# Kernel optimization log

Measured on AMD Instinct MI355X. Metric: run time of the kernel, lower is better.

Reference implementation:

```python
import jax, jax.numpy as jnp
import numpy as np

N_NODES = 100000
N_EDGES = 1000000
NHID = 128
N_CLASSES = 5000


def setup_inputs() -> dict:
    key = jax.random.key(0)
    ks = jax.random.split(key, 8)
    feature = jax.random.normal(ks[0], (N_NODES, NHID), dtype=jnp.float32)
    # Linear weights stored as [in, out] so forward is x @ W + b
    W1 = jax.random.normal(ks[1], (2 * NHID, NHID), dtype=jnp.float32) * (1.0 / np.sqrt(2 * NHID))
    b1 = jnp.zeros((NHID,), dtype=jnp.float32)
    alpha = jnp.full((NHID,), 0.25, dtype=jnp.float32)  # PReLU per-channel init
    W2 = jax.random.normal(ks[2], (NHID, 2), dtype=jnp.float32) * (1.0 / np.sqrt(NHID))
    b2 = jnp.zeros((2,), dtype=jnp.float32)
    row = jax.random.randint(ks[3], (N_EDGES,), 0, N_NODES, dtype=jnp.int64)
    col = jax.random.randint(ks[4], (N_EDGES,), 0, N_NODES, dtype=jnp.int64)
    label = jax.random.randint(ks[5], (N_NODES,), 0, N_CLASSES, dtype=jnp.int64)
    return {"feature": feature, "W1": W1, "b1": b1, "alpha": alpha,
            "W2": W2, "b2": b2, "row": row, "col": col, "label": label}


def reference(feature, W1, b1, alpha, W2, b2, row, col, label):
    # per-edge label: 1 if endpoints share a cluster label
    y = (label[row] == label[col]).astype(jnp.int32)  # [E]
    # edge gather + concat: [E, 2*nhid]
    x = jnp.concatenate([feature[row], feature[col]], axis=1)
    h = x @ W1 + b1                                   # [E, nhid]
    h = jnp.where(h >= 0, h, alpha * h)               # PReLU, per-channel alpha
    logits = h @ W2 + b2                              # [E, 2]
    logp = jax.nn.log_softmax(logits, axis=-1)
    # mean cross-entropy over edges
    loss = -jnp.mean(jnp.take_along_axis(logp, y[:, None], axis=1))
    return loss
```

## Files before the change

kernel.cpp:

```cpp
#include <hip/hip_runtime.h>
#include <hip/hip_bf16.h>

typedef __bf16 bf16_t;
typedef bf16_t bf16x8 __attribute__((ext_vector_type(8)));
typedef float floatx4 __attribute__((ext_vector_type(4)));
typedef float floatx2 __attribute__((ext_vector_type(2)));

#define N_NODES 100000
#define N_EDGES 1000000

#define NBK 98
#define NBP 104
#define NSEG 23
#define SEGCAP 512
#define BCAP (NSEG * SEGCAP)
#define SPCAP 32768
#define SCAT_BLKS 326
#define SCAT_WIN 3072

#define OFF_AUX   12800000
#define OFF_WT    14400000
#define OFF_WABS  14465536
#define OFF_W1G   14466048
#define OFF_CONST 14466560
#define OFF_RS    14466624ULL
#define OFF_SPILL 24264256ULL
#define OFF_CNT   24526400ULL
#define WS_NEED   24533120ULL
#define CNT_INTS  (NBP * 16 + 16)


__global__ __launch_bounds__(256) void k_prep(const float* __restrict__ W1,
                                              const float* __restrict__ b1,
                                              const float* __restrict__ alpha,
                                              const float* __restrict__ W2,
                                              const float* __restrict__ b2,
                                              bf16_t* __restrict__ WT,
                                              float* __restrict__ wabsp,
                                              float* __restrict__ w1g,
                                              float* __restrict__ constg,
                                              float* __restrict__ out,
                                              int* __restrict__ cnt,
                                              int zero_cnt) {
    const int t = threadIdx.x;
    if (blockIdx.x < 128) {
        int i = blockIdx.x * 256 + t;
        int n = i >> 7, k = i & 127;
        float v = (n < 128) ? W1[k * 128 + n] : W1[(k + 128) * 128 + (n - 128)];
        WT[i] = (bf16_t)v;
        return;
    }
    if (zero_cnt) {
        for (int i = t; i < CNT_INTS; i += 256) cnt[i] = 0;
    }
    __shared__ float w1L[128];
    if (t < 128) {
        float wd = W2[2 * t + 1] - W2[2 * t];
        float al = alpha[t];
        float w1v = wd * (1.f + al) * 0.5f;
        w1L[t] = w1v;
        w1g[t] = w1v;
        int col = (t & 64) + (t & 3) * 16 + ((t >> 2) & 15);
        float wdc = W2[2 * col + 1] - W2[2 * col];
        wabsp[t] = wdc * (1.f - alpha[col]) * 0.5f;
    }
    __syncthreads();
    if (t < 64) {
        float c = fmaf(w1L[t], b1[t], w1L[t + 64] * b1[t + 64]);
#pragma unroll
        for (int m = 32; m >= 1; m >>= 1) c += __shfl_xor(c, m, 64);
        if (t == 0) { *constg = c + (b2[1] - b2[0]); out[0] = 0.f; }
    }
}

__device__ inline unsigned fp4_code(float x) {
    float a = fabsf(x);
    unsigned code = (unsigned)(a > 0.25f) + (a > 0.75f) + (a > 1.25f) + (a > 1.75f)
                  + (a > 2.5f) + (a > 3.5f) + (a > 5.0f);
    return code | (x < 0.f ? 8u : 0u);
}

__global__ __launch_bounds__(256) void k_gemm(const float* __restrict__ F,
                                              const bf16_t* __restrict__ WT,
                                              const float* __restrict__ b1,
                                              const float* __restrict__ w1g,
                                              const int* __restrict__ label,
                                              unsigned char* __restrict__ PQ4,
                                              float4* __restrict__ aux_g,
                                              const int* __restrict__ row,
                                              const int* __restrict__ col,
                                              int2* __restrict__ RS,
                                              int2* __restrict__ spill,
                                              int* __restrict__ cnt,
                                              int do_scatter) {
    __shared__ __align__(16) char smem[34176];
    const int t = threadIdx.x;

    if (blockIdx.x < SCAT_BLKS) {
        if (!do_scatter) return;
        int* hist = (int*)smem;
        int* lofs = ((int*)smem) + NBP;
        int* base = ((int*)smem) + 2 * NBP;
        const int w0 = blockIdx.x * SCAT_WIN;
        for (int i = t; i < NBP; i += 256) { hist[i] = 0; lofs[i] = 0; }
        __syncthreads();
        int r[12], c[12];
#pragma unroll
        for (int k = 0; k < 12; ++k) {
            int e = w0 + k * 256 + t;
            int es = (e < N_EDGES) ? e : (N_EDGES - 1);
            r[k] = row[es]; c[k] = col[es];
            if (e < N_EDGES) atomicAdd(&hist[r[k] >> 10], 1);
        }
        __syncthreads();
        for (int b = t; b < NBP; b += 256) {
            int n = hist[b];
            base[b] = n ? atomicAdd(&cnt[b * 16], n) : 0;
        }
        __syncthreads();
#pragma unroll
        for (int k = 0; k < 12; ++k) {
            int e = w0 + k * 256 + t;
            if (e < N_EDGES) {
                int b = r[k] >> 10;
                int lo = atomicAdd(&lofs[b], 1);
                int gp = base[b] + lo;
                if (gp < BCAP) RS[(size_t)b * BCAP + gp] = make_int2(r[k], c[k]);
                else {
                    int sp = atomicAdd(&cnt[NBP * 16], 1);
                    if (sp < SPCAP) spill[sp] = make_int2(r[k], c[k]);
                }
            }
        }
        return;
    }

    bf16x8* Bs = (bf16x8*)smem;
    float (*sP1)[16] = (float (*)[16])(smem + 32768);
    float (*sP2)[16] = (float (*)[16])(smem + 33024);
    const int m0 = (blockIdx.x - SCAT_BLKS) * 32;

    const int w = t >> 6, lane = t & 63;
    const int l15 = lane & 15, quad = lane >> 4;
    const int rw = w >> 1, wq = w & 1;

    const int arow = m0 + rw * 16 + l15;
    const float4* Ar = (const float4*)(F + (size_t)arow * 128 + quad * 8);
    float4 fa[4], fb[4];
#pragma unroll
    for (int s = 0; s < 4; ++s) { fa[s] = Ar[s * 8]; fb[s] = Ar[s * 8 + 1]; }

    float w1v[4], bv[4];
#pragma unroll
    for (int nt = 0; nt < 4; ++nt) {
        int cch = wq * 64 + nt * 16 + l15;
        w1v[nt] = w1g[cch];
        bv[nt] = b1[cch];
    }

    const bf16x8* WT8 = (const bf16x8*)WT;
#pragma unroll
    for (int j = 0; j < 8; ++j) {
        int chunk = j * 256 + t;
        int cr = chunk >> 4, cc = chunk & 15;
        Bs[cr * 16 + (cc ^ (cr & 15))] = WT8[chunk];
    }

    bf16x8 Af[4];
#pragma unroll
    for (int s = 0; s < 4; ++s) {
        bf16x8 v;
        v[0] = (bf16_t)fa[s].x; v[1] = (bf16_t)fa[s].y;
        v[2] = (bf16_t)fa[s].z; v[3] = (bf16_t)fa[s].w;
        v[4] = (bf16_t)fb[s].x; v[5] = (bf16_t)fb[s].y;
        v[6] = (bf16_t)fb[s].z; v[7] = (bf16_t)fb[s].w;
        Af[s] = v;
    }
    __syncthreads();

#pragma unroll
    for (int h = 0; h < 2; ++h) {
        floatx4 acc[4] = {};
#pragma unroll
        for (int s = 0; s < 4; ++s) {
            bf16x8 Bf[4];
#pragma unroll
            for (int nt = 0; nt < 4; ++nt) {
                int cr = wq * 64 + nt * 16 + l15;
                Bf[nt] = Bs[cr * 16 + ((s * 4 + quad) ^ (cr & 15))];
            }
#pragma unroll
            for (int nt = 0; nt < 4; ++nt)
                acc[nt] = __builtin_amdgcn_mfma_f32_16x16x32_bf16(Af[s], Bf[nt], acc[nt], 0, 0, 0);
        }

#pragma unroll
        for (int rr = 0; rr < 4; ++rr) {
            float sv = 0.f;
#pragma unroll
            for (int nt = 0; nt < 4; ++nt) sv = fmaf(w1v[nt], acc[nt][rr], sv);
#pragma unroll
            for (int m = 8; m >= 1; m >>= 1) sv += __shfl_xor(sv, m, 64);
            if (l15 == 0) {
                if (h == 0) sP1[w][quad * 4 + rr] = sv;
                else        sP2[w][quad * 4 + rr] = sv;
            }
        }

#pragma unroll
        for (int rr = 0; rr < 4; ++rr) {
            int g = m0 + rw * 16 + quad * 4 + rr;
            float v0 = acc[0][rr], v1 = acc[1][rr], v2 = acc[2][rr], v3 = acc[3][rr];
            if (h == 0) { v0 += bv[0]; v1 += bv[1]; v2 += bv[2]; v3 += bv[3]; }
            unsigned pk = fp4_code(v0) | (fp4_code(v1) << 4)
                        | (fp4_code(v2) << 8) | (fp4_code(v3) << 12);
            *(unsigned short*)(PQ4 + (size_t)g * 128 + h * 64 + wq * 32 + l15 * 2) =
                (unsigned short)pk;
        }

        if (h == 0) {
            __syncthreads();
#pragma unroll
            for (int j = 0; j < 8; ++j) {
                int chunk = j * 256 + t;
                int cr = chunk >> 4, cc = chunk & 15;
                Bs[cr * 16 + (cc ^ (cr & 15))] = WT8[2048 + chunk];
            }
            __syncthreads();
        }
    }

    __syncthreads();
    if (t < 32) {
        int rw2 = t >> 4, ri = t & 15;
        float s1 = sP1[rw2 * 2][ri] + sP1[rw2 * 2 + 1][ri];
        float s2 = sP2[rw2 * 2][ri] + sP2[rw2 * 2 + 1][ri];
        int g = m0 + rw2 * 16 + ri;
        float4 av = {s1, s2, __int_as_float(label[g]), 0.f};
        aux_g[g] = av;
    }
}

__device__ inline void fp4_decode(unsigned d, unsigned& pe, unsigned& po) {
    unsigned ne = d & 0x0F0F0F0Fu;
    unsigned no = (d >> 4) & 0x0F0F0F0Fu;
    pe = __builtin_amdgcn_perm(0x4C484440u, 0x3C383000u, ne & 0x07070707u)
       | ((ne & 0x08080808u) << 4);
    po = __builtin_amdgcn_perm(0x4C484440u, 0x3C383000u, no & 0x07070707u)
       | ((no & 0x08080808u) << 4);
}

template <int B>
__device__ inline float dw_pair(unsigned p, unsigned q, const float (&W)[32]) {
    unsigned pe, po, qe, qo;
    fp4_decode(p, pe, po);
    fp4_decode(q, qe, qo);
    floatx2 he0 = __builtin_amdgcn_cvt_pk_f32_fp8((int)pe, false)
                + __builtin_amdgcn_cvt_pk_f32_fp8((int)qe, false);
    floatx2 he1 = __builtin_amdgcn_cvt_pk_f32_fp8((int)pe, true)
                + __builtin_amdgcn_cvt_pk_f32_fp8((int)qe, true);
    floatx2 ho0 = __builtin_amdgcn_cvt_pk_f32_fp8((int)po, false)
                + __builtin_amdgcn_cvt_pk_f32_fp8((int)qo, false);
    floatx2 ho1 = __builtin_amdgcn_cvt_pk_f32_fp8((int)po, true)
                + __builtin_amdgcn_cvt_pk_f32_fp8((int)qo, true);
    float s;
    s = fabsf(he0[0]) * W[B + 0];
    s = fmaf(fabsf(he0[1]), W[B + 1], s);
    s = fmaf(fabsf(he1[0]), W[B + 2], s);
    s = fmaf(fabsf(he1[1]), W[B + 3], s);
    s = fmaf(fabsf(ho0[0]), W[B + 4], s);
    s = fmaf(fabsf(ho0[1]), W[B + 5], s);
    s = fmaf(fabsf(ho1[0]), W[B + 6], s);
    s = fmaf(fabsf(ho1[1]), W[B + 7], s);
    return s;
}

__global__ __launch_bounds__(256) void k_edge_bkt(const unsigned char* __restrict__ PQ4,
                                                  const float4* __restrict__ aux,
                                                  const float* __restrict__ wabsp,
                                                  const float* __restrict__ constg,
                                                  const int2* __restrict__ RS,
                                                  const int2* __restrict__ spill,
                                                  const int* __restrict__ cnt,
                                                  float* __restrict__ out) {
    const int lane = threadIdx.x & 63;
    const int w = threadIdx.x >> 6;
    const int sub = lane & 3, eidx = lane >> 2;

    const int2* seg; int segN;
    {
        const int blk = blockIdx.x;
        if (blk < NBP * NSEG) {
            int bk = blk % NBP, sg = blk / NBP;
            int cc = cnt[bk * 16]; if (cc > BCAP) cc = BCAP;
            int st = sg * SEGCAP;
            segN = cc - st; if (segN < 0) segN = 0; if (segN > SEGCAP) segN = SEGCAP;
            seg = RS + (size_t)bk * BCAP + st;
        } else {
            int sc = cnt[NBP * 16]; if (sc > SPCAP) sc = SPCAP;
            int si = blk - NBP * NSEG;
            int per = (sc + 7) >> 3;
            int st = si * per;
            segN = sc - st; if (segN < 0) segN = 0; if (segN > per) segN = per;
            seg = spill + st;
        }
    }

    float W[32];
    const float* wb = wabsp + sub * 32;
#pragma unroll
    for (int d = 0; d < 4; ++d) {
        const float* wd = wb + d * 8;
        W[d * 8 + 0] = wd[0]; W[d * 8 + 1] = wd[2];
        W[d * 8 + 2] = wd[4]; W[d * 8 + 3] = wd[6];
        W[d * 8 + 4] = wd[1]; W[d * 8 + 5] = wd[3];
        W[d * 8 + 6] = wd[5]; W[d * 8 + 7] = wd[7];
    }
    const float CB = *constg;

    float acc = 0.f;
    for (int base = w * 64; base < segN; base += 256) {
        int sl = base + lane;
        if (sl >= segN) sl = segN - 1;
        int2 rc = seg[sl];
        int rowreg = rc.x, colreg = rc.y;

        int rV[4], cV[4];
#pragma unroll
        for (int c = 0; c < 4; ++c) {
            rV[c] = __shfl(rowreg, c * 16 + eidx, 64);
            cV[c] = __shfl(colreg, c * 16 + eidx, 64);
        }
        int alow = ((lane >> 5) << 4) + (lane & 15);
        int ra1 = __shfl(rowreg, alow, 64), ca1 = __shfl(colreg, alow, 64);
        int ra2 = __shfl(rowreg, 32 + alow, 64), ca2 = __shfl(colreg, 32 + alow, 64);
        int n1 = (lane & 16) ? ca1 : ra1;
        int n2 = (lane & 16) ? ca2 : ra2;
        float4 A1 = aux[n1];
        float4 A2 = aux[n2];

        uint4 P[4], Q[4];
#pragma unroll
        for (int c = 0; c < 4; ++c) {
            P[c] = *(const uint4*)(PQ4 + (unsigned)rV[c] * 128u + (unsigned)sub * 16u);
            Q[c] = *(const uint4*)(PQ4 + (unsigned)cV[c] * 128u + 64u + (unsigned)sub * 16u);
        }

#pragma unroll
        for (int c = 0; c < 4; ++c) {
            float s = dw_pair<0>(P[c].x, Q[c].x, W)
                    + dw_pair<8>(P[c].y, Q[c].y, W)
                    + dw_pair<16>(P[c].z, Q[c].z, W)
                    + dw_pair<24>(P[c].w, Q[c].w, W);
            s += __shfl_xor(s, 1, 64);
            s += __shfl_xor(s, 2, 64);
            const float4 Av = (c < 2) ? A1 : A2;
            const int bs = (c & 1) * 32;
            float s1 = __shfl(Av.x, bs + eidx, 64);
            float s2 = __shfl(Av.y, bs + 16 + eidx, 64);
            float lr = __shfl(Av.z, bs + eidx, 64);
            float lc = __shfl(Av.z, bs + 16 + eidx, 64);
            float D = s1 + s2 + CB + s;
            float sgn = (__float_as_int(lr) == __float_as_int(lc)) ? -D : D;
            float loss = fmaxf(sgn, 0.f) + __logf(1.f + __expf(-fabsf(sgn)));
            acc += (sub == 0 && (base + c * 16 + eidx) < segN) ? loss : 0.f;
        }
    }

#pragma unroll
    for (int m = 32; m >= 1; m >>= 1) acc += __shfl_xor(acc, m, 64);
    __shared__ float sdata[4];
    if (lane == 0) sdata[w] = acc;
    __syncthreads();
    if (threadIdx.x == 0) {
        float ssum = (sdata[0] + sdata[1]) + (sdata[2] + sdata[3]);
        atomicAdd(out, ssum * (1.f / (float)N_EDGES));
    }
}

__global__ __launch_bounds__(256) void k_edge_loss(const unsigned char* __restrict__ PQ4,
                                                   const float4* __restrict__ aux,
                                                   const float* __restrict__ wabsp,
                                                   const float* __restrict__ constg,
                                                   const int* __restrict__ row,
                                                   const int* __restrict__ col,
                                                   float* __restrict__ out) {
    const int lane = threadIdx.x & 63;
    const int wid = (blockIdx.x * blockDim.x + threadIdx.x) >> 6;
    const int e0 = wid * 64;
    const int sub = lane & 3, eidx = lane >> 2;

    float W[32];
    const float* wb = wabsp + sub * 32;
#pragma unroll
    for (int d = 0; d < 4; ++d) {
        const float* wd = wb + d * 8;
        W[d * 8 + 0] = wd[0]; W[d * 8 + 1] = wd[2];
        W[d * 8 + 2] = wd[4]; W[d * 8 + 3] = wd[6];
        W[d * 8 + 4] = wd[1]; W[d * 8 + 5] = wd[3];
        W[d * 8 + 6] = wd[5]; W[d * 8 + 7] = wd[7];
    }
    const float CB = *constg;

    int el = e0 + lane;
    if (el >= N_EDGES) el = N_EDGES - 1;
    int rowreg = row[el];
    int colreg = col[el];

    int rV[4], cV[4];
#pragma unroll
    for (int c = 0; c < 4; ++c) {
        rV[c] = __shfl(rowreg, c * 16 + eidx, 64);
        cV[c] = __shfl(colreg, c * 16 + eidx, 64);
    }
    int alow = ((lane >> 5) << 4) + (lane & 15);
    int ra1 = __shfl(rowreg, alow, 64), ca1 = __shfl(colreg, alow, 64);
    int ra2 = __shfl(rowreg, 32 + alow, 64), ca2 = __shfl(colreg, 32 + alow, 64);
    int n1 = (lane & 16) ? ca1 : ra1;
    int n2 = (lane & 16) ? ca2 : ra2;
    float4 A1 = aux[n1];
    float4 A2 = aux[n2];

    uint4 P[4], Q[4];
#pragma unroll
    for (int c = 0; c < 4; ++c) {
        P[c] = *(const uint4*)(PQ4 + (unsigned)rV[c] * 128u + (unsigned)sub * 16u);
        Q[c] = *(const uint4*)(PQ4 + (unsigned)cV[c] * 128u + 64u + (unsigned)sub * 16u);
    }
    __builtin_amdgcn_sched_barrier(0);

    float acc = 0.f;
#pragma unroll
    for (int c = 0; c < 4; ++c) {
        float s = dw_pair<0>(P[c].x, Q[c].x, W)
                + dw_pair<8>(P[c].y, Q[c].y, W)
                + dw_pair<16>(P[c].z, Q[c].z, W)
                + dw_pair<24>(P[c].w, Q[c].w, W);
        s += __shfl_xor(s, 1, 64);
        s += __shfl_xor(s, 2, 64);
        const float4 Av = (c < 2) ? A1 : A2;
        const int base = (c & 1) * 32;
        float s1 = __shfl(Av.x, base + eidx, 64);
        float s2 = __shfl(Av.y, base + 16 + eidx, 64);
        float lr = __shfl(Av.z, base + eidx, 64);
        float lc = __shfl(Av.z, base + 16 + eidx, 64);
        float D = s1 + s2 + CB + s;
        float sgn = (__float_as_int(lr) == __float_as_int(lc)) ? -D : D;
        float loss = fmaxf(sgn, 0.f) + __logf(1.f + __expf(-fabsf(sgn)));
        int e = e0 + c * 16 + eidx;
        acc += (sub == 0 && e < N_EDGES) ? loss : 0.f;
    }

#pragma unroll
    for (int m = 32; m >= 1; m >>= 1) acc += __shfl_xor(acc, m, 64);
    __shared__ float sdata[4];
    int l64 = threadIdx.x & 63;
    int wv = threadIdx.x >> 6;
    if (l64 == 0) sdata[wv] = acc;
    __syncthreads();
    if (threadIdx.x == 0) {
        float ssum = (sdata[0] + sdata[1]) + (sdata[2] + sdata[3]);
        atomicAdd(out, ssum * (1.f / (float)N_EDGES));
    }
}

extern "C" void kernel_launch(void* const* d_in, const int* in_sizes, int n_in,
                              void* d_out, int out_size, void* d_ws, size_t ws_size,
                              hipStream_t stream) {
    const float* feature = (const float*)d_in[0];
    const float* W1      = (const float*)d_in[1];
    const float* b1      = (const float*)d_in[2];
    const float* alpha   = (const float*)d_in[3];
    const float* W2      = (const float*)d_in[4];
    const float* b2      = (const float*)d_in[5];
    const int*   row     = (const int*)d_in[6];
    const int*   col     = (const int*)d_in[7];
    const int*   label   = (const int*)d_in[8];
    float* out = (float*)d_out;

    char* ws = (char*)d_ws;
    unsigned char* PQ4 = (unsigned char*)(ws);
    float* aux   = (float*)(ws + OFF_AUX);
    bf16_t* WT   = (bf16_t*)(ws + OFF_WT);
    float* wabsp = (float*)(ws + OFF_WABS);
    float* w1g   = (float*)(ws + OFF_W1G);
    float* constg= (float*)(ws + OFF_CONST);

    const int bkt = (ws_size >= WS_NEED) ? 1 : 0;
    int2* RS    = (int2*)(ws + (bkt ? OFF_RS    : 0));
    int2* spill = (int2*)(ws + (bkt ? OFF_SPILL : 0));
    int*  cnt   = (int*)(ws + (bkt ? OFF_CNT    : 0));

    k_prep<<<129, 256, 0, stream>>>(W1, b1, alpha, W2, b2, WT, wabsp, w1g,
                                    constg, out, cnt, bkt);
    k_gemm<<<SCAT_BLKS + 3125, 256, 0, stream>>>(feature, WT, b1, w1g, label,
                                                 PQ4, (float4*)aux, row, col,
                                                 RS, spill, cnt, bkt);
    if (bkt) {
        k_edge_bkt<<<NBP * NSEG + 8, 256, 0, stream>>>(PQ4, (const float4*)aux,
                                                       wabsp, constg, RS, spill,
                                                       cnt, out);
    } else {
        k_edge_loss<<<3907, 256, 0, stream>>>(PQ4, (const float4*)aux, wabsp,
                                              constg, row, col, out);
    }
}
```

Baseline: 183.0 us.

## Software-pipeline bucketed edge loop with prefetched index and gather loads

Restructures the bucketed edge kernel so each wave handles 16 edges per iteration, interleaved across the four waves. Index pairs are prefetched two iterations ahead and feature/aux gathers one iteration ahead, with a sched_barrier keeping the loads issued before the compute of the current iteration. Each lane now loads the index pair directly instead of broadcasting it through many shuffles, which aims to hide gather latency and remove the shuffle overhead. In exchange, each iteration covers fewer edges, so there is more loop overhead and more live registers for the double-buffered data.

Result: no change. 182.7 us (-0.2%).

```diff
diff --git a/kernel.cpp b/kernel.cpp
--- a/kernel.cpp
+++ b/kernel.cpp
@@ -275,6 +275,38 @@
     return s;
 }
 
+__device__ inline int2 ldRS(const int2* __restrict__ seg, int off, int lane,
+                            int segN) {
+    int ei = off + (lane >> 2);
+    ei = (ei < segN) ? ei : (segN - 1);
+    return seg[ei];
+}
+
+__device__ inline void ldG(const unsigned char* __restrict__ PQ4,
+                           const float4* __restrict__ aux, int2 rc, int sub,
+                           uint4& P, uint4& Q, float4& A) {
+    P = *(const uint4*)(PQ4 + (unsigned)rc.x * 128u + (unsigned)sub * 16u);
+    Q = *(const uint4*)(PQ4 + (unsigned)rc.y * 128u + 64u + (unsigned)sub * 16u);
+    A = aux[(sub & 1) ? rc.y : rc.x];
+}
+
+__device__ inline float edge16(uint4 P, uint4 Q, float4 A, int off, int segN,
+                               int lane, int sub, const float (&W)[32],
+                               float CB) {
+    float s = dw_pair<0>(P.x, Q.x, W) + dw_pair<8>(P.y, Q.y, W)
+            + dw_pair<16>(P.z, Q.z, W) + dw_pair<24>(P.w, Q.w, W);
+    s += __shfl_xor(s, 1, 64);
+    s += __shfl_xor(s, 2, 64);
+    int gb = lane & ~3;
+    float s2 = __shfl(A.y, gb + 1, 64);
+    float lc = __shfl(A.z, gb + 1, 64);
+    float D = A.x + s2 + CB + s;
+    float sgn = (__float_as_int(A.z) == __float_as_int(lc)) ? -D : D;
+    float loss = fmaxf(sgn, 0.f) + __logf(1.f + __expf(-fabsf(sgn)));
+    bool valid = (sub == 0) && (off + (lane >> 2) < segN);
+    return valid ? loss : 0.f;
+}
+
 __global__ __launch_bounds__(256) void k_edge_bkt(const unsigned char* __restrict__ PQ4,
                                                   const float4* __restrict__ aux,
                                                   const float* __restrict__ wabsp,
@@ -285,7 +317,7 @@
                                                   float* __restrict__ out) {
     const int lane = threadIdx.x & 63;
     const int w = threadIdx.x >> 6;
-    const int sub = lane & 3, eidx = lane >> 2;
+    const int sub = lane & 3;
 
     const int2* seg; int segN;
     {
@@ -318,59 +350,31 @@
     }
     const float CB = *constg;
 
-    float acc = 0.f;
-    for (int base = w * 64; base < segN; base += 256) {
-        int sl = base + lane;
-        if (sl >= segN) sl = segN - 1;
-        int2 rc = seg[sl];
-        int rowreg = rc.x, colreg = rc.y;
-
-        int rV[4], cV[4];
-#pragma unroll
-        for (int c = 0; c < 4; ++c) {
-            rV[c] = __shfl(rowreg, c * 16 + eidx, 64);
-            cV[c] = __shfl(colreg, c * 16 + eidx, 64);
-        }
-        int alow = ((lane >> 5) << 4) + (lane & 15);
-        int ra1 = __shfl(rowreg, alow, 64), ca1 = __shfl(colreg, alow, 64);
-        int ra2 = __shfl(rowreg, 32 + alow, 64), ca2 = __shfl(colreg, 32 + alow, 64);
-        int n1 = (lane & 16) ? ca1 : ra1;
-        int n2 = (lane & 16) ? ca2 : ra2;
-        float4 A1 = aux[n1];
-        float4 A2 = aux[n2];
-
-        uint4 P[4], Q[4];
-#pragma unroll
-        for (int c = 0; c < 4; ++c) {
-            P[c] = *(const uint4*)(PQ4 + (unsigned)rV[c] * 128u + (unsigned)sub * 16u);
-            Q[c] = *(const uint4*)(PQ4 + (unsigned)cV[c] * 128u + 64u + (unsigned)sub * 16u);
-        }
-
-#pragma unroll
-        for (int c = 0; c < 4; ++c) {
-            float s = dw_pair<0>(P[c].x, Q[c].x, W)
-                    + dw_pair<8>(P[c].y, Q[c].y, W)
-                    + dw_pair<16>(P[c].z, Q[c].z, W)
-                    + dw_pair<24>(P[c].w, Q[c].w, W);
-            s += __shfl_xor(s, 1, 64);
-            s += __shfl_xor(s, 2, 64);
-            const float4 Av = (c < 2) ? A1 : A2;
-            const int bs = (c & 1) * 32;
-            float s1 = __shfl(Av.x, bs + eidx, 64);
-            float s2 = __shfl(Av.y, bs + 16 + eidx, 64);
-            float lr = __shfl(Av.z, bs + eidx, 64);
-            float lc = __shfl(Av.z, bs + 16 + eidx, 64);
-            float D = s1 + s2 + CB + s;
-            float sgn = (__float_as_int(lr) == __float_as_int(lc)) ? -D : D;
-            float loss = fmaxf(sgn, 0.f) + __logf(1.f + __expf(-fabsf(sgn)));
-            acc += (sub == 0 && (base + c * 16 + eidx) < segN) ? loss : 0.f;
-        }
-    }
-
-#pragma unroll
-    for (int m = 32; m >= 1; m >>= 1) acc += __shfl_xor(acc, m, 64);
+    const int off0 = w * 16;
+    const int nMy = (segN > off0) ? ((segN - off0 + 63) >> 6) : 0;
+    float accw = 0.f;
+    if (nMy > 0) {
+        int2 rcCur = ldRS(seg, off0, lane, segN);
+        int2 rcNext = (nMy > 1) ? ldRS(seg, off0 + 64, lane, segN) : rcCur;
+        uint4 Pc, Qc; float4 Ac;
+        ldG(PQ4, aux, rcCur, sub, Pc, Qc, Ac);
+        for (int k = 0; k < nMy; ++k) {
+            int2 rcN2 = (k + 2 < nMy) ? ldRS(seg, off0 + (k + 2) * 64, lane, segN)
+                                      : rcCur;
+            uint4 Pn, Qn; float4 An;
+            int2 rcG = (k + 1 < nMy) ? rcNext : rcCur;
+            ldG(PQ4, aux, rcG, sub, Pn, Qn, An);
+            __builtin_amdgcn_sched_barrier(0);
+            accw += edge16(Pc, Qc, Ac, off0 + k * 64, segN, lane, sub, W, CB);
+            rcCur = rcNext; rcNext = rcN2;
+            Pc = Pn; Qc = Qn; Ac = An;
+        }
+    }
+
+#pragma unroll
+    for (int m = 32; m >= 1; m >>= 1) accw += __shfl_xor(accw, m, 64);
     __shared__ float sdata[4];
-    if (lane == 0) sdata[w] = acc;
+    if (lane == 0) sdata[w] = accw;
     __syncthreads();
     if (threadIdx.x == 0) {
         float ssum = (sdata[0] + sdata[1]) + (sdata[2] + sdata[3]);
```
